# Kernel optimization log

Hardware: AMD Instinct MI355X
Metric: run time of the kernel (lower is better)

## Reference

```python
import jax, jax.numpy as jnp
import numpy as np

B, T, D = 2, 1024, 6144
NQ, NKV, HD = 48, 8, 128          # q heads, kv heads, head dim
MULT = 0.08838834764831845        # attn_output_multiplier = 1/sqrt(128)
MAX_ATTN = 30.0                   # tanh logit cap
ROPE_BASE = 10000.0


def rotate_half(x):
    x1, x2 = jnp.split(x, 2, axis=-1)
    return jnp.concatenate((-x2, x1), axis=-1)


def rope(x):
    # x: [b, s, h, d]; offset = 0 (no kv memory)
    d = x.shape[-1]
    exponents = jnp.arange(0, d, 2, dtype=jnp.float32)
    inv_freq = 1.0 / (ROPE_BASE ** (exponents / d))
    t = jnp.arange(x.shape[1], dtype=jnp.float32)[None, :]          # [1, s]
    phase = jnp.einsum('bi,j->bij', t, inv_freq)                    # [1, s, d/2]
    phase = jnp.tile(phase, reps=(1, 2))[:, :, None, :]             # [1, s, 1, d]
    return (x * jnp.cos(phase) + rotate_half(x) * jnp.sin(phase)).astype(x.dtype)


def setup_inputs() -> dict:
    key = jax.random.key(0)
    ks = jax.random.split(key, 8)
    s = 0.02
    return {
        'query': jax.random.normal(ks[0], (B, T, D), jnp.float32),
        'key':   jax.random.normal(ks[1], (B, T, D), jnp.float32),
        'value': jax.random.normal(ks[2], (B, T, D), jnp.float32),
        'mask':  jnp.tril(jnp.ones((1, 1, T, T), dtype=bool)),
        'wq': jax.random.normal(ks[3], (D, NQ * HD), jnp.float32) * s,
        'bq': jnp.zeros((NQ * HD,), jnp.float32),
        'wk': jax.random.normal(ks[4], (D, NKV * HD), jnp.float32) * s,
        'bk': jnp.zeros((NKV * HD,), jnp.float32),
        'wv': jax.random.normal(ks[5], (D, NKV * HD), jnp.float32) * s,
        'bv': jnp.zeros((NKV * HD,), jnp.float32),
        'wo': jax.random.normal(ks[6], (NQ * HD, D), jnp.float32) * s,
    }


def reference(query, key, value, mask, wq, bq, wk, bk, wv, bv, wo):
    def proj(x, w, b, n_heads):
        y = x @ w + b
        return y.reshape(x.shape[0], x.shape[1], n_heads, HD)

    q = rope(proj(query, wq, bq, NQ))    # [b, t, 48, 128]
    k = rope(proj(key,   wk, bk, NKV))   # [b, T, 8, 128]
    v = proj(value, wv, bv, NKV)         # [b, T, 8, 128]

    b, t, h, d = q.shape
    q = q.reshape(b, t, NKV, h // NKV, d)                      # [b, t, 8, 6, 128]

    logits = jnp.einsum('bthHd,bThd->bhHtT', q, k).astype(jnp.float32)
    logits = logits * MULT
    logits = MAX_ATTN * jnp.tanh(logits / MAX_ATTN)            # soft logit cap
    m = mask[:, :, None, :, :]                                 # [1, 1, 1, t, T]
    logits = jnp.where(m, logits, -1e30)
    attn_w = jax.nn.softmax(logits, axis=-1).astype(query.dtype)

    attn = jnp.einsum('bhHtT,bThd->bthHd', attn_w, v)          # [b, t, 8, 6, 128]
    attn = attn.reshape(b, t, -1)                              # [b, t, 6144]
    return attn @ wo                                           # final proj, no bias
```

## Files before the change

### kernel.cpp

```cpp
#include <hip/hip_runtime.h>
#include <hip/hip_bf16.h>

#define B_ 2
#define T_ 1024
#define D_ 6144
#define NQ_ 48
#define NKV_ 8
#define HD_ 128
#define GQ_ 6
#define MULT_ 0.08838834764831845f
#define MAXATTN_ 30.0f

typedef __bf16 bf8_t __attribute__((ext_vector_type(8)));
typedef short short8 __attribute__((ext_vector_type(8)));
typedef float f4 __attribute__((ext_vector_type(4)));

__device__ inline float b2f(unsigned short u) {
  return __uint_as_float(((unsigned int)u) << 16);
}
__device__ inline unsigned short f2b(float f) {
  unsigned int u = __float_as_uint(f);
  u += 0x7FFFu + ((u >> 16) & 1u);
  return (unsigned short)(u >> 16);
}
__device__ inline bf8_t ld_frag(const unsigned short* p) {
  return __builtin_bit_cast(bf8_t, *reinterpret_cast<const short8*>(p));
}
__device__ inline f4 mfma16x16(bf8_t a, bf8_t b, f4 c) {
  return __builtin_amdgcn_mfma_f32_16x16x32_bf16(a, b, c, 0, 0, 0);
}
__device__ __forceinline__ void gld_lds16(const void* g, void* l) {
  __builtin_amdgcn_global_load_lds(
      (__attribute__((address_space(1))) void*)g,
      (__attribute__((address_space(3))) void*)l, 16, 0, 0);
}

__global__ __launch_bounds__(256) void conv_bf16_k(
    const float* __restrict__ x, unsigned short* __restrict__ y)
{
  size_t i = (size_t)blockIdx.x * 256 + threadIdx.x;
  const f4* xv = (const f4*)x;
  f4 a = xv[2 * i], b = xv[2 * i + 1];
  short8 o;
  #pragma unroll
  for (int j = 0; j < 4; ++j) {
    o[j] = (short)f2b(a[j]);
    o[4 + j] = (short)f2b(b[j]);
  }
  *((short8*)y + i) = o;
}

__global__ __launch_bounds__(256) void transpose_w_k(
    const float* __restrict__ W, unsigned short* __restrict__ Wt, int K, int N)
{
  __shared__ float t[64][33];
  const int nb = blockIdx.x * 32;
  const int kb = blockIdx.y * 64;
  const int tx = threadIdx.x;
  const int ty = threadIdx.y;
  #pragma unroll
  for (int j = ty; j < 64; j += 8)
    t[j][tx] = W[(size_t)(kb + j) * N + nb + tx];
  __syncthreads();
  #pragma unroll
  for (int j = ty; j < 32; j += 8) {
    unsigned int pk = (unsigned int)f2b(t[2 * tx][j]) |
                      ((unsigned int)f2b(t[2 * tx + 1][j]) << 16);
    *reinterpret_cast<unsigned int*>(&Wt[(size_t)(nb + j) * K + kb + 2 * tx]) = pk;
  }
}

template <int OUT_F32, int BN>
__device__ __forceinline__ void gemm_bt_body(
    const unsigned short* __restrict__ A, const unsigned short* __restrict__ Bt,
    const float* __restrict__ bias, void* __restrict__ Cp,
    int N, int K, int m0, int n0)
{
  constexpr int WN = BN / 2;
  constexpr int FB = BN / 32;
  constexpr int RB = BN / 64;
  __shared__ unsigned short As[128 * 32];
  __shared__ unsigned short Bs[BN * 32];
  const int tid = threadIdx.x;
  const int wave = tid >> 6;
  const int lane = tid & 63;
  const int quad = lane >> 4;
  const int l16 = lane & 15;
  const int wr = wave >> 1;
  const int wc = wave & 1;
  const int srow = tid >> 2;
  const int skc = (tid & 3) * 8;

  f4 acc[4][FB];
  #pragma unroll
  for (int i = 0; i < 4; ++i)
    #pragma unroll
    for (int j = 0; j < FB; ++j) acc[i][j] = f4{0.f, 0.f, 0.f, 0.f};

  for (int k0 = 0; k0 < K; k0 += 32) {
    #pragma unroll
    for (int r = 0; r < 2; ++r)
      gld_lds16(A + (size_t)(m0 + r * 64 + srow) * K + k0 + skc,
                &As[(r * 256 + wave * 64) * 8]);
    #pragma unroll
    for (int r = 0; r < RB; ++r)
      gld_lds16(Bt + (size_t)(n0 + r * 64 + srow) * K + k0 + skc,
                &Bs[(r * 256 + wave * 64) * 8]);
    __syncthreads();
    bf8_t af[4], bfr[FB];
    #pragma unroll
    for (int i = 0; i < 4; ++i)
      af[i] = ld_frag(&As[(wr * 64 + i * 16 + l16) * 32 + quad * 8]);
    #pragma unroll
    for (int j = 0; j < FB; ++j)
      bfr[j] = ld_frag(&Bs[(wc * WN + j * 16 + l16) * 32 + quad * 8]);
    #pragma unroll
    for (int i = 0; i < 4; ++i)
      #pragma unroll
      for (int j = 0; j < FB; ++j)
        acc[i][j] = mfma16x16(af[i], bfr[j], acc[i][j]);
    __syncthreads();
  }

  #pragma unroll
  for (int j = 0; j < FB; ++j) {
    const int gn = n0 + wc * WN + j * 16 + l16;
    const float bv = bias ? bias[gn] : 0.f;
    #pragma unroll
    for (int i = 0; i < 4; ++i) {
      #pragma unroll
      for (int r = 0; r < 4; ++r) {
        const int gm = m0 + wr * 64 + i * 16 + quad * 4 + r;
        const float v = acc[i][j][r] + bv;
        if constexpr (OUT_F32)
          ((float*)Cp)[(size_t)gm * N + gn] = v;
        else
          ((unsigned short*)Cp)[(size_t)gm * N + gn] = f2b(v);
      }
    }
  }
}

template <int OUT_F32, int BN>
__global__ __launch_bounds__(256) void gemm_bt_k(
    const unsigned short* __restrict__ A, const unsigned short* __restrict__ Bt,
    const float* __restrict__ bias, void* __restrict__ Cp, int N, int K)
{
  gemm_bt_body<OUT_F32, BN>(A, Bt, bias, Cp, N, K,
                            blockIdx.y * 128, blockIdx.x * BN);
}

__global__ __launch_bounds__(256) void gemm_kv_k(
    const unsigned short* __restrict__ Ak, const unsigned short* __restrict__ Av,
    const unsigned short* __restrict__ Btk, const unsigned short* __restrict__ Btv,
    const float* __restrict__ bk, const float* __restrict__ bv,
    unsigned short* __restrict__ Ck, unsigned short* __restrict__ Cv,
    int N, int K)
{
  const bool z = (blockIdx.z != 0);
  gemm_bt_body<0, 64>(z ? Av : Ak, z ? Btv : Btk, z ? bv : bk,
                      z ? (void*)Cv : (void*)Ck, N, K,
                      blockIdx.y * 128, blockIdx.x * 64);
}

__global__ __launch_bounds__(256) void rope_k(unsigned short* __restrict__ X,
                                              int nheads, int total)
{
  int idx = blockIdx.x * 256 + threadIdx.x;
  if (idx >= total) return;
  int i = idx & 63;
  int rem = idx >> 6;
  int t = (rem / nheads) % T_;
  size_t base = (size_t)rem * HD_;
  float inv = expf(-9.210340371976184f * (float)(2 * i) * (1.0f / 128.0f));
  float ph = (float)t * inv;
  float sp, cp;
  sincosf(ph, &sp, &cp);
  float x1 = b2f(X[base + i]);
  float x2 = b2f(X[base + 64 + i]);
  X[base + i]      = f2b(x1 * cp - x2 * sp);
  X[base + 64 + i] = f2b(x2 * cp + x1 * sp);
}

__global__ __launch_bounds__(256) void attn_k(
    const unsigned short* __restrict__ Q,
    const unsigned short* __restrict__ Kb,
    const unsigned short* __restrict__ Vb,
    unsigned short* __restrict__ O)
{
  __shared__ unsigned short Pls[4][16][32];
  const int tid = threadIdx.x;
  const int wave = tid >> 6;
  const int lane = tid & 63;
  const int quad = lane >> 4;
  const int l16 = lane & 15;
  const int b = blockIdx.z;
  const int h = blockIdx.y;
  const int hk = h / GQ_;
  const int t0 = blockIdx.x * 64 + wave * 16;

  bf8_t qf[4];
  {
    const unsigned short* qp =
        Q + ((size_t)(b * T_ + t0 + l16) * NQ_ + h) * HD_ + quad * 8;
    #pragma unroll
    for (int i = 0; i < 4; i++) qf[i] = ld_frag(qp + i * 32);
  }

  f4 accO[8];
  #pragma unroll
  for (int i = 0; i < 8; i++) accO[i] = f4{0.f, 0.f, 0.f, 0.f};
  float mrow[4] = {-1e30f, -1e30f, -1e30f, -1e30f};
  float lrow[4] = {0.f, 0.f, 0.f, 0.f};

  const int kend = t0 + 16;
  for (int t1 = 0; t1 < kend; t1 += 32) {
    f4 s0 = f4{0.f,0.f,0.f,0.f}, s1 = f4{0.f,0.f,0.f,0.f};
    {
      const unsigned short* kp0 =
          Kb + ((size_t)(b * T_ + t1 + l16) * NKV_ + hk) * HD_ + quad * 8;
      const unsigned short* kp1 = kp0 + 16 * NKV_ * HD_;
      #pragma unroll
      for (int i = 0; i < 4; i++) {
        s0 = mfma16x16(qf[i], ld_frag(kp0 + i * 32), s0);
        s1 = mfma16x16(qf[i], ld_frag(kp1 + i * 32), s1);
      }
    }
    #pragma unroll
    for (int r = 0; r < 4; r++) {
      int qg = t0 + quad * 4 + r;
      float v0 = s0[r] * MULT_;
      float v1 = s1[r] * MULT_;
      v0 = MAXATTN_ * tanhf(v0 * (1.0f / MAXATTN_));
      v1 = MAXATTN_ * tanhf(v1 * (1.0f / MAXATTN_));
      if (t1 + l16 > qg)      v0 = -1e30f;
      if (t1 + 16 + l16 > qg) v1 = -1e30f;
      float tmax = fmaxf(v0, v1);
      #pragma unroll
      for (int off = 1; off < 16; off <<= 1)
        tmax = fmaxf(tmax, __shfl_xor(tmax, off, 16));
      float mnew = fmaxf(mrow[r], tmax);
      float alpha = __expf(mrow[r] - mnew);
      float p0 = __expf(v0 - mnew);
      float p1 = __expf(v1 - mnew);
      float ps = p0 + p1;
      #pragma unroll
      for (int off = 1; off < 16; off <<= 1)
        ps += __shfl_xor(ps, off, 16);
      lrow[r] = lrow[r] * alpha + ps;
      mrow[r] = mnew;
      #pragma unroll
      for (int nt = 0; nt < 8; nt++) accO[nt][r] *= alpha;
      Pls[wave][quad * 4 + r][l16]      = f2b(p0);
      Pls[wave][quad * 4 + r][16 + l16] = f2b(p1);
    }
    __threadfence_block();
    bf8_t pfrag = ld_frag(&Pls[wave][l16][quad * 8]);
    const unsigned short* vp =
        Vb + ((size_t)(b * T_ + t1) * NKV_ + hk) * HD_ + l16;
    #pragma unroll
    for (int nt = 0; nt < 8; nt++) {
      short8 vv;
      #pragma unroll
      for (int j = 0; j < 8; j++)
        vv[j] = (short)vp[(size_t)(quad * 8 + j) * (NKV_ * HD_) + nt * 16];
      accO[nt] = mfma16x16(pfrag, __builtin_bit_cast(bf8_t, vv), accO[nt]);
    }
  }

  float invl[4];
  #pragma unroll
  for (int r = 0; r < 4; r++) invl[r] = 1.0f / lrow[r];
  #pragma unroll
  for (int nt = 0; nt < 8; nt++) {
    #pragma unroll
    for (int r = 0; r < 4; r++) {
      int tg = t0 + quad * 4 + r;
      O[((size_t)(b * T_ + tg) * NQ_ + h) * HD_ + nt * 16 + l16] =
          f2b(accO[nt][r] * invl[r]);
    }
  }
}

extern "C" void kernel_launch(void* const* d_in, const int* in_sizes, int n_in,
                              void* d_out, int out_size, void* d_ws, size_t ws_size,
                              hipStream_t stream)
{
  const float* q_in = (const float*)d_in[0];
  const float* k_in = (const float*)d_in[1];
  const float* v_in = (const float*)d_in[2];
  const float* wq = (const float*)d_in[4];
  const float* bq = (const float*)d_in[5];
  const float* wk = (const float*)d_in[6];
  const float* bk = (const float*)d_in[7];
  const float* wv = (const float*)d_in[8];
  const float* bv = (const float*)d_in[9];
  const float* wo = (const float*)d_in[10];

  char* ws = (char*)d_ws;
  unsigned short* WT  = (unsigned short*)(ws);
  unsigned short* WKt = (unsigned short*)(ws + 75497472);
  unsigned short* WVt = (unsigned short*)(ws + 88080384);
  unsigned short* Ab  = (unsigned short*)(ws + 75497472);
  unsigned short* Qb  = (unsigned short*)(ws + 100663296);
  unsigned short* Kb  = (unsigned short*)(ws + 125829120);
  unsigned short* Vb  = (unsigned short*)(ws + 130023424);
  unsigned short* Xq  = (unsigned short*)d_out;
  unsigned short* Xk  = (unsigned short*)d_out;
  unsigned short* Xv  = (unsigned short*)d_out + 12582912;

  dim3 blk(256);
  dim3 tb(32, 8);

  conv_bf16_k<<<6144, blk, 0, stream>>>(q_in, Xq);
  transpose_w_k<<<dim3(192, 96), tb, 0, stream>>>(wq, WT, D_, NQ_ * HD_);
  transpose_w_k<<<dim3(32, 96), tb, 0, stream>>>(wk, WKt, D_, NKV_ * HD_);
  transpose_w_k<<<dim3(32, 96), tb, 0, stream>>>(wv, WVt, D_, NKV_ * HD_);

  gemm_bt_k<0, 128><<<dim3(48, 16), blk, 0, stream>>>(
      Xq, WT, bq, Qb, NQ_ * HD_, D_);

  conv_bf16_k<<<6144, blk, 0, stream>>>(k_in, Xk);
  conv_bf16_k<<<6144, blk, 0, stream>>>(v_in, Xv);
  transpose_w_k<<<dim3(192, 96), tb, 0, stream>>>(wo, WT, NQ_ * HD_, D_);

  gemm_kv_k<<<dim3(16, 16, 2), blk, 0, stream>>>(
      Xk, Xv, WKt, WVt, bk, bv, Kb, Vb, NKV_ * HD_, D_);

  rope_k<<<(B_ * T_ * NQ_ * 64) / 256, blk, 0, stream>>>(
      Qb, NQ_, B_ * T_ * NQ_ * 64);
  rope_k<<<(B_ * T_ * NKV_ * 64) / 256, blk, 0, stream>>>(
      Kb, NKV_, B_ * T_ * NKV_ * 64);

  attn_k<<<dim3(T_ / 64, NQ_, B_), blk, 0, stream>>>(Qb, Kb, Vb, Ab);

  gemm_bt_k<1, 128><<<dim3(48, 16), blk, 0, stream>>>(
      Ab, WT, nullptr, d_out, D_, NQ_ * HD_);
}
```

Before: 1.351 ms.

## Transpose V in GEMM epilogue, use fixed-max softmax, balance causal tiles

The V projection epilogue now writes V transposed as [b, kv-head, d, t]. The attention kernel can then load V fragments as contiguous 16-byte vectors instead of eight scalar strided gathers. Because the tanh cap bounds logits by 30, the online softmax drops its running max, rescaling and per-step shuffles, and computes exp(capped-30) in closed form with a single final row-sum reduction. Each block now processes a mirrored pair of query tiles (one late, one early) to even out causal work across blocks, halving the grid. The fixed-max trick relies on the cap bound; very negative values may underflow, which matches the reference up to rounding.

Result: faster. 1.256 ms (-7.0%).

```diff
diff --git a/kernel.cpp b/kernel.cpp
--- a/kernel.cpp
+++ b/kernel.cpp
@@ -13,6 +13,7 @@
 
 typedef __bf16 bf8_t __attribute__((ext_vector_type(8)));
 typedef short short8 __attribute__((ext_vector_type(8)));
+typedef short short4v __attribute__((ext_vector_type(4)));
 typedef float f4 __attribute__((ext_vector_type(4)));
 
 __device__ inline float b2f(unsigned short u) {
@@ -70,7 +71,7 @@
   }
 }
 
-template <int OUT_F32, int BN>
+template <int OUT, int BN>
 __device__ __forceinline__ void gemm_bt_body(
     const unsigned short* __restrict__ A, const unsigned short* __restrict__ Bt,
     const float* __restrict__ bias, void* __restrict__ Cp,
@@ -125,42 +126,53 @@
   #pragma unroll
   for (int j = 0; j < FB; ++j) {
     const int gn = n0 + wc * WN + j * 16 + l16;
-    const float bv = bias ? bias[gn] : 0.f;
+    const float bv = (OUT == 1) ? (bias ? bias[gn] : 0.f) : bias[gn];
     #pragma unroll
     for (int i = 0; i < 4; ++i) {
-      #pragma unroll
-      for (int r = 0; r < 4; ++r) {
-        const int gm = m0 + wr * 64 + i * 16 + quad * 4 + r;
-        const float v = acc[i][j][r] + bv;
-        if constexpr (OUT_F32)
-          ((float*)Cp)[(size_t)gm * N + gn] = v;
-        else
-          ((unsigned short*)Cp)[(size_t)gm * N + gn] = f2b(v);
+      if constexpr (OUT == 2) {
+        const int gm0 = m0 + wr * 64 + i * 16 + quad * 4;
+        const int bb = gm0 >> 10;
+        const int tt = gm0 & 1023;
+        short4v pk;
+        #pragma unroll
+        for (int r = 0; r < 4; ++r) pk[r] = (short)f2b(acc[i][j][r] + bv);
+        *reinterpret_cast<short4v*>(
+            &((unsigned short*)Cp)[((size_t)(bb * 1024 + gn)) * 1024 + tt]) = pk;
+      } else {
+        #pragma unroll
+        for (int r = 0; r < 4; ++r) {
+          const int gm = m0 + wr * 64 + i * 16 + quad * 4 + r;
+          const float v = acc[i][j][r] + bv;
+          if constexpr (OUT == 1)
+            ((float*)Cp)[(size_t)gm * N + gn] = v;
+          else
+            ((unsigned short*)Cp)[(size_t)gm * N + gn] = f2b(v);
+        }
       }
     }
   }
 }
 
-template <int OUT_F32, int BN>
+template <int OUT, int BN>
 __global__ __launch_bounds__(256) void gemm_bt_k(
     const unsigned short* __restrict__ A, const unsigned short* __restrict__ Bt,
     const float* __restrict__ bias, void* __restrict__ Cp, int N, int K)
 {
-  gemm_bt_body<OUT_F32, BN>(A, Bt, bias, Cp, N, K,
-                            blockIdx.y * 128, blockIdx.x * BN);
+  gemm_bt_body<OUT, BN>(A, Bt, bias, Cp, N, K,
+                        blockIdx.y * 128, blockIdx.x * BN);
 }
 
 __global__ __launch_bounds__(256) void gemm_kv_k(
     const unsigned short* __restrict__ Ak, const unsigned short* __restrict__ Av,
     const unsigned short* __restrict__ Btk, const unsigned short* __restrict__ Btv,
     const float* __restrict__ bk, const float* __restrict__ bv,
-    unsigned short* __restrict__ Ck, unsigned short* __restrict__ Cv,
+    unsigned short* __restrict__ Ck, unsigned short* __restrict__ Cvt,
     int N, int K)
 {
-  const bool z = (blockIdx.z != 0);
-  gemm_bt_body<0, 64>(z ? Av : Ak, z ? Btv : Btk, z ? bv : bk,
-                      z ? (void*)Cv : (void*)Ck, N, K,
-                      blockIdx.y * 128, blockIdx.x * 64);
+  if (blockIdx.z == 0)
+    gemm_bt_body<0, 64>(Ak, Btk, bk, Ck, N, K, blockIdx.y * 128, blockIdx.x * 64);
+  else
+    gemm_bt_body<2, 64>(Av, Btv, bv, Cvt, N, K, blockIdx.y * 128, blockIdx.x * 64);
 }
 
 __global__ __launch_bounds__(256) void rope_k(unsigned short* __restrict__ X,
@@ -182,23 +194,12 @@
   X[base + 64 + i] = f2b(x2 * cp + x1 * sp);
 }
 
-__global__ __launch_bounds__(256) void attn_k(
-    const unsigned short* __restrict__ Q,
-    const unsigned short* __restrict__ Kb,
-    const unsigned short* __restrict__ Vb,
-    unsigned short* __restrict__ O)
-{
-  __shared__ unsigned short Pls[4][16][32];
-  const int tid = threadIdx.x;
-  const int wave = tid >> 6;
-  const int lane = tid & 63;
-  const int quad = lane >> 4;
-  const int l16 = lane & 15;
-  const int b = blockIdx.z;
-  const int h = blockIdx.y;
-  const int hk = h / GQ_;
-  const int t0 = blockIdx.x * 64 + wave * 16;
-
+__device__ __forceinline__ void attn_qtile(
+    const unsigned short* __restrict__ Q, const unsigned short* __restrict__ Kb,
+    const unsigned short* __restrict__ Vt, unsigned short* __restrict__ O,
+    unsigned short* __restrict__ Pw,
+    int b, int h, int hk, int t0, int quad, int l16)
+{
   bf8_t qf[4];
   {
     const unsigned short* qp =
@@ -210,9 +211,9 @@
   f4 accO[8];
   #pragma unroll
   for (int i = 0; i < 8; i++) accO[i] = f4{0.f, 0.f, 0.f, 0.f};
-  float mrow[4] = {-1e30f, -1e30f, -1e30f, -1e30f};
-  float lrow[4] = {0.f, 0.f, 0.f, 0.f};
-
+  float lpart[4] = {0.f, 0.f, 0.f, 0.f};
+
+  const unsigned short* vbase = Vt + (size_t)(b * NKV_ + hk) * HD_ * T_;
   const int kend = t0 + 16;
   for (int t1 = 0; t1 < kend; t1 += 32) {
     f4 s0 = f4{0.f,0.f,0.f,0.f}, s1 = f4{0.f,0.f,0.f,0.f};
@@ -228,58 +229,66 @@
     }
     #pragma unroll
     for (int r = 0; r < 4; r++) {
-      int qg = t0 + quad * 4 + r;
-      float v0 = s0[r] * MULT_;
-      float v1 = s1[r] * MULT_;
-      v0 = MAXATTN_ * tanhf(v0 * (1.0f / MAXATTN_));
-      v1 = MAXATTN_ * tanhf(v1 * (1.0f / MAXATTN_));
-      if (t1 + l16 > qg)      v0 = -1e30f;
-      if (t1 + 16 + l16 > qg) v1 = -1e30f;
-      float tmax = fmaxf(v0, v1);
-      #pragma unroll
-      for (int off = 1; off < 16; off <<= 1)
-        tmax = fmaxf(tmax, __shfl_xor(tmax, off, 16));
-      float mnew = fmaxf(mrow[r], tmax);
-      float alpha = __expf(mrow[r] - mnew);
-      float p0 = __expf(v0 - mnew);
-      float p1 = __expf(v1 - mnew);
-      float ps = p0 + p1;
-      #pragma unroll
-      for (int off = 1; off < 16; off <<= 1)
-        ps += __shfl_xor(ps, off, 16);
-      lrow[r] = lrow[r] * alpha + ps;
-      mrow[r] = mnew;
-      #pragma unroll
-      for (int nt = 0; nt < 8; nt++) accO[nt][r] *= alpha;
-      Pls[wave][quad * 4 + r][l16]      = f2b(p0);
-      Pls[wave][quad * 4 + r][16 + l16] = f2b(p1);
+      const int qg = t0 + quad * 4 + r;
+      float e0 = __expf(s0[r] * (2.f * MULT_ / MAXATTN_));
+      float e1 = __expf(s1[r] * (2.f * MULT_ / MAXATTN_));
+      float p0 = __expf(-2.f * MAXATTN_ * __builtin_amdgcn_rcpf(e0 + 1.f));
+      float p1 = __expf(-2.f * MAXATTN_ * __builtin_amdgcn_rcpf(e1 + 1.f));
+      if (t1 + l16 > qg)      p0 = 0.f;
+      if (t1 + 16 + l16 > qg) p1 = 0.f;
+      lpart[r] += p0 + p1;
+      Pw[(quad * 4 + r) * 32 + l16]      = f2b(p0);
+      Pw[(quad * 4 + r) * 32 + 16 + l16] = f2b(p1);
     }
     __threadfence_block();
-    bf8_t pfrag = ld_frag(&Pls[wave][l16][quad * 8]);
-    const unsigned short* vp =
-        Vb + ((size_t)(b * T_ + t1) * NKV_ + hk) * HD_ + l16;
+    bf8_t pfrag = ld_frag(&Pw[l16 * 32 + quad * 8]);
     #pragma unroll
     for (int nt = 0; nt < 8; nt++) {
-      short8 vv;
-      #pragma unroll
-      for (int j = 0; j < 8; j++)
-        vv[j] = (short)vp[(size_t)(quad * 8 + j) * (NKV_ * HD_) + nt * 16];
-      accO[nt] = mfma16x16(pfrag, __builtin_bit_cast(bf8_t, vv), accO[nt]);
+      bf8_t vf = ld_frag(vbase + (size_t)(nt * 16 + l16) * T_ + t1 + quad * 8);
+      accO[nt] = mfma16x16(pfrag, vf, accO[nt]);
     }
   }
 
   float invl[4];
   #pragma unroll
-  for (int r = 0; r < 4; r++) invl[r] = 1.0f / lrow[r];
+  for (int r = 0; r < 4; r++) {
+    float s = lpart[r];
+    #pragma unroll
+    for (int off = 1; off < 16; off <<= 1) s += __shfl_xor(s, off, 16);
+    invl[r] = __builtin_amdgcn_rcpf(s);
+  }
   #pragma unroll
   for (int nt = 0; nt < 8; nt++) {
     #pragma unroll
     for (int r = 0; r < 4; r++) {
-      int tg = t0 + quad * 4 + r;
+      const int tg = t0 + quad * 4 + r;
       O[((size_t)(b * T_ + tg) * NQ_ + h) * HD_ + nt * 16 + l16] =
           f2b(accO[nt][r] * invl[r]);
     }
   }
+}
+
+__global__ __launch_bounds__(256) void attn_k(
+    const unsigned short* __restrict__ Q,
+    const unsigned short* __restrict__ Kb,
+    const unsigned short* __restrict__ Vt,
+    unsigned short* __restrict__ O)
+{
+  __shared__ unsigned short Pls[4][16][32];
+  const int tid = threadIdx.x;
+  const int wave = tid >> 6;
+  const int lane = tid & 63;
+  const int quad = lane >> 4;
+  const int l16 = lane & 15;
+  const int b = blockIdx.z;
+  const int h = blockIdx.y;
+  const int hk = h / GQ_;
+  unsigned short* Pw = &Pls[wave][0][0];
+
+  const int xa = blockIdx.x;
+  const int xh = (T_ / 64 - 1) - xa;
+  attn_qtile(Q, Kb, Vt, O, Pw, b, h, hk, xh * 64 + wave * 16, quad, l16);
+  attn_qtile(Q, Kb, Vt, O, Pw, b, h, hk, xa * 64 + wave * 16, quad, l16);
 }
 
 extern "C" void kernel_launch(void* const* d_in, const int* in_sizes, int n_in,
@@ -304,7 +313,7 @@
   unsigned short* Ab  = (unsigned short*)(ws + 75497472);
   unsigned short* Qb  = (unsigned short*)(ws + 100663296);
   unsigned short* Kb  = (unsigned short*)(ws + 125829120);
-  unsigned short* Vb  = (unsigned short*)(ws + 130023424);
+  unsigned short* Vt  = (unsigned short*)(ws + 130023424);
   unsigned short* Xq  = (unsigned short*)d_out;
   unsigned short* Xk  = (unsigned short*)d_out;
   unsigned short* Xv  = (unsigned short*)d_out + 12582912;
@@ -325,14 +334,14 @@
   transpose_w_k<<<dim3(192, 96), tb, 0, stream>>>(wo, WT, NQ_ * HD_, D_);
 
   gemm_kv_k<<<dim3(16, 16, 2), blk, 0, stream>>>(
-      Xk, Xv, WKt, WVt, bk, bv, Kb, Vb, NKV_ * HD_, D_);
+      Xk, Xv, WKt, WVt, bk, bv, Kb, Vt, NKV_ * HD_, D_);
 
   rope_k<<<(B_ * T_ * NQ_ * 64) / 256, blk, 0, stream>>>(
       Qb, NQ_, B_ * T_ * NQ_ * 64);
   rope_k<<<(B_ * T_ * NKV_ * 64) / 256, blk, 0, stream>>>(
       Kb, NKV_, B_ * T_ * NKV_ * 64);
 
-  attn_k<<<dim3(T_ / 64, NQ_, B_), blk, 0, stream>>>(Qb, Kb, Vb, Ab);
+  attn_k<<<dim3(T_ / 128, NQ_, B_), blk, 0, stream>>>(Qb, Kb, Vt, Ab);
 
   gemm_bt_k<1, 128><<<dim3(48, 16), blk, 0, stream>>>(
       Ab, WT, nullptr, d_out, D_, NQ_ * HD_);
```
